# Optimization experiments

Hardware: AMD Instinct MI355X
Metric: run time of the kernel (lower is better)

The kernel has to match this reference:

```python
import jax, jax.numpy as jnp
import numpy as np

N_SAMPLES = 8192
EMBED_DIM = 128
NUM_CLASSES = 100


def setup_inputs() -> dict:
    key = jax.random.key(0)
    k1, k2 = jax.random.split(key)
    x = jax.random.normal(k1, (N_SAMPLES, EMBED_DIM), dtype=jnp.float32)
    # FastAP assumes L2-normalized embeddings (dist2 = 2 - 2*cos in [0, 4])
    x = x / jnp.linalg.norm(x, axis=1, keepdims=True)
    labels = jax.random.randint(k2, (N_SAMPLES,), 0, NUM_CLASSES, dtype=jnp.int64 if jax.config.jax_enable_x64 else jnp.int32)
    return {"batch": x, "labels": labels, "num_bins": 10}


def reference(batch, labels, num_bins):
    N = batch.shape[0]
    L = num_bins + 1                      # number of histogram bin centers (edges of linspace)
    Delta = 4.0 / num_bins                # bin width
    Z = jnp.linspace(0.0, 4.0, L)

    same = labels[:, None] == labels[None, :]
    eye = jnp.eye(N, dtype=bool)
    I_pos = (same & ~eye).astype(batch.dtype)   # Aff > 0
    I_neg = (~same).astype(batch.dtype)         # Aff < 0 (diag is 'same', so excluded)
    N_pos = I_pos.sum(axis=1)

    # squared euclidean distance for unit-norm rows: 2 - 2*cos
    dist2 = 2.0 - 2.0 * (batch @ batch.T)       # [N, N]

    # soft-binning histogram: one N x N pulse per bin, reduced to per-row counts.
    # lax.map keeps only one [N, N] pulse buffer alive at a time.
    def bin_fn(z):
        pulse = jnp.maximum(0.0, 1.0 - jnp.abs(dist2 - z) / Delta)
        return (jnp.einsum('ij,ij->i', pulse, I_pos),
                jnp.einsum('ij,ij->i', pulse, I_neg))

    hp, hn = jax.lax.map(bin_fn, Z)             # each [L, N]
    h_pos = hp.T                                # [N, L]
    h_neg = hn.T

    H_pos = jnp.cumsum(h_pos, axis=1)
    H = jnp.cumsum(h_pos + h_neg, axis=1)

    # FastAP = h_pos * H_pos / H, with NaN/Inf (H == 0) zeroed, as in the original
    safe_H = jnp.where(H > 0, H, 1.0)
    ap = jnp.where(H > 0, h_pos * H_pos / safe_H, 0.0).sum(axis=1)

    # divide by N_pos; rows with no positives are dropped from the mean
    valid = N_pos > 0
    safe_Np = jnp.where(valid, N_pos, 1.0)
    ap = jnp.where(valid, ap / safe_Np, 0.0)

    n_valid = valid.sum().astype(batch.dtype)
    loss = 1.0 - ap.sum() / n_valid
    return loss
```

## Files before the change

kernel.cpp:

```cpp
#include <hip/hip_runtime.h>

#define NS 8192
#define EMBED 128
#define ROWCHUNK 512
#define NPANEL (ROWCHUNK / 32)
#define AROW 12
#define INV64K (1.0f / 65536.0f)

typedef __bf16 bf16x8 __attribute__((ext_vector_type(8)));
typedef float f32x4 __attribute__((ext_vector_type(4)));
typedef float f32x2 __attribute__((ext_vector_type(2)));
typedef const __attribute__((address_space(1))) unsigned ag_u32;
typedef __attribute__((address_space(3))) unsigned al_u32;

#define OFF_XB  0u
#define OFF_GS  2097152u
#define OFF_GSP 2228224u
#define OFF_GA  2359296u
#define OFF_GAP 2752512u
#define OFF_DB  3145728u
#define OFF_AC  3146240u
#define ZERO_BYTES 1049104u

__device__ inline unsigned short f2bf(float f) {
  unsigned u = __float_as_uint(f);
  u += 0x7fffu + ((u >> 16) & 1u);
  return (unsigned short)(u >> 16);
}
__device__ inline float clamp01(float x) { return __builtin_amdgcn_fmed3f(x, 0.f, 1.f); }

__global__ __launch_bounds__(256) void prep_kernel(const float* __restrict__ x,
                                                   unsigned short* __restrict__ xb,
                                                   uint4* __restrict__ zbase) {
  const int gid = blockIdx.x * 256 + threadIdx.x;
  const int row = gid >> 4, g = gid & 15;
  const float4 v0 = reinterpret_cast<const float4*>(x)[row * 32 + g * 2];
  const float4 v1 = reinterpret_cast<const float4*>(x)[row * 32 + g * 2 + 1];
  uint4 o;
  o.x = (unsigned)f2bf(v0.x) | ((unsigned)f2bf(v0.y) << 16);
  o.y = (unsigned)f2bf(v0.z) | ((unsigned)f2bf(v0.w) << 16);
  o.z = (unsigned)f2bf(v1.x) | ((unsigned)f2bf(v1.y) << 16);
  o.w = (unsigned)f2bf(v1.z) | ((unsigned)f2bf(v1.w) << 16);
  reinterpret_cast<uint4*>(xb)[row * 16 + (g ^ (row & 7))] = o;
  if (gid < (int)(ZERO_BYTES / 16u)) zbase[gid] = make_uint4(0u, 0u, 0u, 0u);
}

__global__ __launch_bounds__(256, 8) void fastap_main_kernel(
    const unsigned short* __restrict__ xb,
    const int* __restrict__ labels,
    unsigned* __restrict__ gS, unsigned* __restrict__ gSp,
    unsigned* __restrict__ gA, unsigned* __restrict__ gAp,
    unsigned* __restrict__ doneBx,
    float* __restrict__ accum, unsigned* __restrict__ done,
    float* __restrict__ out) {
  __shared__ __align__(16) unsigned short sA[2][32 * 128];
  __shared__ int sLab[ROWCHUNK];
  __shared__ int sFinal;

  const int tid  = threadIdx.x;
  const int wave = tid >> 6;
  const int lane = tid & 63;
  const int l16  = lane & 15;
  const int quad = lane >> 4;
  const int colBase  = blockIdx.x * 64;
  const int rowChunk = blockIdx.y * ROWCHUNK;

  if (tid < ROWCHUNK / 4)
    reinterpret_cast<int4*>(sLab)[tid] =
        reinterpret_cast<const int4*>(labels + rowChunk)[tid];

  const int jcol = colBase + wave * 16 + l16;
  bf16x8 bfr[4];
  #pragma unroll
  for (int kb = 0; kb < 4; ++kb) {
    const int pg = (kb * 4 + quad) ^ (l16 & 7);
    bfr[kb] = *reinterpret_cast<const bf16x8*>(&xb[jcol * 128 + pg * 8]);
  }
  const int labj = labels[jcol];

  f32x2 C01 = {0.f, 0.f}, C23 = {0.f, 0.f};
  f32x2 Cp01 = {0.f, 0.f}, Cp23 = {0.f, 0.f};

  int aOff[4];
  #pragma unroll
  for (int kb = 0; kb < 4; ++kb)
    aOff[kb] = l16 * 128 + (((kb * 4 + quad) ^ (l16 & 7)) << 3);

  const unsigned short* xrb = xb + rowChunk * 128;
  auto stage = [&](int p, int b) {
    const unsigned short* src = xrb + p * (32 * 128);
    __builtin_amdgcn_global_load_lds((ag_u32*)(src + tid * 8),
                                     (al_u32*)(&sA[b][tid * 8]), 16, 0, 0);
    __builtin_amdgcn_global_load_lds((ag_u32*)(src + (tid + 256) * 8),
                                     (al_u32*)(&sA[b][(tid + 256) * 8]), 16, 0, 0);
  };

  auto tile16 = [&](const unsigned short* ap, int lcr) {
    const int4 lr = *reinterpret_cast<const int4*>(&sLab[lcr + quad * 4]);
    bf16x8 a0 = *reinterpret_cast<const bf16x8*>(&ap[aOff[0]]);
    bf16x8 a1 = *reinterpret_cast<const bf16x8*>(&ap[aOff[1]]);
    bf16x8 a2 = *reinterpret_cast<const bf16x8*>(&ap[aOff[2]]);
    bf16x8 a3 = *reinterpret_cast<const bf16x8*>(&ap[aOff[3]]);
    f32x4 acc = {0.f, 0.f, 0.f, 0.f};
    acc = __builtin_amdgcn_mfma_f32_16x16x32_bf16(a0, bfr[0], acc, 0, 0, 0);
    acc = __builtin_amdgcn_mfma_f32_16x16x32_bf16(a1, bfr[1], acc, 0, 0, 0);
    acc = __builtin_amdgcn_mfma_f32_16x16x32_bf16(a2, bfr[2], acc, 0, 0, 0);
    acc = __builtin_amdgcn_mfma_f32_16x16x32_bf16(a3, bfr[3], acc, 0, 0, 0);

    const int labr[4] = {lr.x, lr.y, lr.z, lr.w};
    #pragma unroll
    for (int r = 0; r < 4; ++r) {
      const float a = acc[r];
      const float pm = (labr[r] == labj) ? 1.f : 0.f;
      const f32x2 av = {a, a}, p2 = {pm, pm};
      f32x2 d01 = __builtin_elementwise_fma(av, (f32x2){5.f, 5.f},
                                            (f32x2){-1.f, 0.f});
      f32x2 d23 = __builtin_elementwise_fma(av, (f32x2){5.f, 5.f},
                                            (f32x2){1.f, 2.f});
      d01 = (f32x2){clamp01(d01.x), clamp01(d01.y)};
      d23 = (f32x2){clamp01(d23.x), clamp01(d23.y)};
      C01 += d01; C23 += d23;
      Cp01 = __builtin_elementwise_fma(p2, d01, Cp01);
      Cp23 = __builtin_elementwise_fma(p2, d23, Cp23);
    }

    const float mabs = fmaxf(fmaxf(fabsf(acc[0]), fabsf(acc[1])),
                             fmaxf(fabsf(acc[2]), fabsf(acc[3])));
    if (__builtin_expect(mabs > 0.4f, 0)) {
      #pragma unroll
      for (int r = 0; r < 4; ++r) {
        const float a = acc[r];
        if (fabsf(a) <= 0.4f) continue;
        const int i = rowChunk + lcr + quad * 4 + r;
        const float d0 = clamp01(fmaf(a, 5.f, -1.f));
        const float d1 = clamp01(a * 5.f);
        const float d2 = clamp01(fmaf(a, 5.f, 1.f));
        const float d3 = clamp01(fmaf(a, 5.f, 2.f));
        if (i == jcol) {
          C01 -= (f32x2){d0, d1};  C23 -= (f32x2){d2, d3};
          Cp01 -= (f32x2){d0, d1}; Cp23 -= (f32x2){d2, d3};
          #pragma unroll
          for (int k = 7; k <= 10; ++k)
            atomicAdd(&gA[jcol * AROW + k], (unsigned)(-65536));
        } else {
          const bool isPos = (labr[r] == labj);
          const float t = fmaf(a, -5.f, 5.f);
          #pragma unroll
          for (int k = 0; k <= 2; ++k) {
            const float v = clamp01((float)(k + 1) - t);
            const int q = (int)(v * 65536.f + 0.5f);
            if (q) {
              atomicAdd(&gA[jcol * AROW + k], (unsigned)q);
              if (isPos) atomicAdd(&gAp[jcol * AROW + k], (unsigned)q);
            }
          }
          #pragma unroll
          for (int k = 7; k <= 10; ++k) {
            const float v = clamp01((float)(k + 1) - t) - 1.f;
            const int q = (int)(v * 65536.f - 0.5f);
            if (q) {
              atomicAdd(&gA[jcol * AROW + k], (unsigned)q);
              if (isPos) atomicAdd(&gAp[jcol * AROW + k], (unsigned)q);
            }
          }
        }
      }
    }
  };

  stage(0, 0);
  __syncthreads();

  #pragma unroll 1
  for (int p = 0; p < NPANEL; ++p) {
    const int cur = p & 1;
    if (p + 1 < NPANEL) stage(p + 1, cur ^ 1);
    tile16(&sA[cur][0],        p * 32);
    tile16(&sA[cur][16 * 128], p * 32 + 16);
    __syncthreads();
  }

  #pragma unroll
  for (int m = 16; m < 64; m <<= 1) {
    C01.x  += __shfl_xor(C01.x,  m, 64); C01.y  += __shfl_xor(C01.y,  m, 64);
    C23.x  += __shfl_xor(C23.x,  m, 64); C23.y  += __shfl_xor(C23.y,  m, 64);
    Cp01.x += __shfl_xor(Cp01.x, m, 64); Cp01.y += __shfl_xor(Cp01.y, m, 64);
    Cp23.x += __shfl_xor(Cp23.x, m, 64); Cp23.y += __shfl_xor(Cp23.y, m, 64);
  }

  if (quad == 0) {
    const float Cv[4]  = {C01.x, C01.y, C23.x, C23.y};
    const float Cpv[4] = {Cp01.x, Cp01.y, Cp23.x, Cp23.y};
    #pragma unroll
    for (int k = 0; k < 4; ++k) {
      atomicAdd(&gS[jcol * 4 + k],  (unsigned)(int)lrintf(Cv[k]  * 65536.f));
      atomicAdd(&gSp[jcol * 4 + k], (unsigned)(int)lrintf(Cpv[k] * 65536.f));
    }
  }

  __syncthreads();
  if (tid == 0) {
    __asm__ volatile("" ::: "memory");
    sFinal = (atomicAdd(&doneBx[blockIdx.x], 1u) == 15u);
  }
  __syncthreads();
  if (!sFinal) return;

  if (tid < 128) sLab[tid] = 0;
  __syncthreads();
  for (int idx = tid; idx < NS; idx += 256)
    atomicAdd(&sLab[labels[idx]], 1);
  __syncthreads();

  if (tid < 64) {
    const int col = colBase + tid;
    const int np = sLab[labels[col]] - 1;

    unsigned gsv[4], gspv[4], gav[11], gapv[11];
    #pragma unroll
    for (int k = 0; k < 4; ++k) {
      gsv[k]  = atomicAdd(&gS[col * 4 + k], 0u);
      gspv[k] = atomicAdd(&gSp[col * 4 + k], 0u);
    }
    #pragma unroll
    for (int b = 0; b < 11; ++b) {
      gav[b]  = atomicAdd(&gA[col * AROW + b], 0u);
      gapv[b] = atomicAdd(&gAp[col * AROW + b], 0u);
    }

    float ap = 0.f, val = 0.f, HpPrev = 0.f;
    #pragma unroll
    for (int b = 0; b <= 10; ++b) {
      const float baseH  = (b < 3) ? 0.f
                         : (b < 7) ? (float)(int)gsv[b - 3]  * INV64K : 8192.f;
      const float basePp = (b < 3) ? 0.f
                         : (b < 7) ? (float)(int)gspv[b - 3] * INV64K : (float)np;
      const float H  = baseH  + (float)(int)gav[b]  * INV64K;
      const float Hp = basePp + (float)(int)gapv[b] * INV64K;
      const float hp = Hp - HpPrev;
      HpPrev = Hp;
      if (H > 1e-6f) ap += hp * Hp / H;
    }
    if (np > 0) { ap /= (float)np; val = 1.f; } else ap = 0.f;

    #pragma unroll
    for (int m = 1; m < 64; m <<= 1) {
      ap  += __shfl_xor(ap,  m, 64);
      val += __shfl_xor(val, m, 64);
    }
    if (tid == 0) {
      atomicAdd(&accum[0], ap);
      atomicAdd(&accum[1], val);
      __builtin_amdgcn_s_waitcnt(0);
      __asm__ volatile("" ::: "memory");
      const unsigned prev = atomicAdd(done, 1u);
      if (prev == 127u) {
        const float a2 = atomicAdd(&accum[0], 0.f);
        const float c2 = atomicAdd(&accum[1], 0.f);
        out[0] = 1.f - (c2 > 0.f ? a2 / c2 : 0.f);
      }
    }
  }
}

extern "C" void kernel_launch(void* const* d_in, const int* in_sizes, int n_in,
                              void* d_out, int out_size, void* d_ws, size_t ws_size,
                              hipStream_t stream) {
  const float* x      = (const float*)d_in[0];
  const int*   labels = (const int*)d_in[1];
  float* out = (float*)d_out;

  char* ws = (char*)d_ws;
  unsigned short* xb = (unsigned short*)(ws + OFF_XB);
  unsigned* gS    = (unsigned*)(ws + OFF_GS);
  unsigned* gSp   = (unsigned*)(ws + OFF_GSP);
  unsigned* gA    = (unsigned*)(ws + OFF_GA);
  unsigned* gAp   = (unsigned*)(ws + OFF_GAP);
  unsigned* dBx   = (unsigned*)(ws + OFF_DB);
  float*    accum = (float*)(ws + OFF_AC);
  unsigned* done  = (unsigned*)(ws + OFF_AC + 8);

  prep_kernel<<<512, 256, 0, stream>>>(x, xb, (uint4*)(ws + OFF_GS));
  fastap_main_kernel<<<dim3(NS / 64, NS / ROWCHUNK), 256, 0, stream>>>(
      xb, labels, gS, gSp, gA, gAp, dBx, accum, done, out);
}
```

Baseline: 113.8 us.

## Replace global atomics for cumulative sums with per-rowchunk partial stores

Each block now writes its per-column cumulative bin partials as plain 8-byte stores into a per-row-chunk slot. The last block for a column group sums the 16 slots itself, so the integer atomic accumulation is gone. Per-column-block label counts are built in shared memory during the main loop and added into a small global table, which removes the final block's full 8192-label histogram pass. Finalization loads become relaxed atomic loads instead of atomicAdd(0). The cost is a larger workspace and 16 extra loads per column in the tail.

```diff
diff --git a/kernel.cpp b/kernel.cpp
--- a/kernel.cpp
+++ b/kernel.cpp
@@ -15,12 +15,13 @@
 
 #define OFF_XB  0u
 #define OFF_GS  2097152u
-#define OFF_GSP 2228224u
-#define OFF_GA  2359296u
-#define OFF_GAP 2752512u
-#define OFF_DB  3145728u
-#define OFF_AC  3146240u
-#define ZERO_BYTES 1049104u
+#define OFF_GSP 4194304u
+#define OFF_GA  6291456u
+#define OFF_GAP 6684672u
+#define OFF_CS  7077888u
+#define OFF_DB  7143424u
+#define OFF_AC  7143936u
+#define ZERO_BYTES 852496u
 
 __device__ inline unsigned short f2bf(float f) {
   unsigned u = __float_as_uint(f);
@@ -28,6 +29,23 @@
   return (unsigned short)(u >> 16);
 }
 __device__ inline float clamp01(float x) { return __builtin_amdgcn_fmed3f(x, 0.f, 1.f); }
+
+__device__ inline void st8_dev(float* p, float x, float y) {
+  unsigned long long u =
+      ((unsigned long long)__float_as_uint(y) << 32) | __float_as_uint(x);
+  __hip_atomic_store(reinterpret_cast<unsigned long long*>(p), u,
+                     __ATOMIC_RELAXED, __HIP_MEMORY_SCOPE_AGENT);
+}
+__device__ inline float2 ld8_dev(const float* p) {
+  unsigned long long u =
+      __hip_atomic_load(reinterpret_cast<const unsigned long long*>(p),
+                        __ATOMIC_RELAXED, __HIP_MEMORY_SCOPE_AGENT);
+  return make_float2(__uint_as_float((unsigned)u),
+                     __uint_as_float((unsigned)(u >> 32)));
+}
+__device__ inline unsigned ld4_dev(const unsigned* p) {
+  return __hip_atomic_load(p, __ATOMIC_RELAXED, __HIP_MEMORY_SCOPE_AGENT);
+}
 
 __global__ __launch_bounds__(256) void prep_kernel(const float* __restrict__ x,
                                                    unsigned short* __restrict__ xb,
@@ -48,13 +66,14 @@
 __global__ __launch_bounds__(256, 8) void fastap_main_kernel(
     const unsigned short* __restrict__ xb,
     const int* __restrict__ labels,
-    unsigned* __restrict__ gS, unsigned* __restrict__ gSp,
+    float* __restrict__ gS, float* __restrict__ gSp,
     unsigned* __restrict__ gA, unsigned* __restrict__ gAp,
-    unsigned* __restrict__ doneBx,
+    unsigned* __restrict__ ccS, unsigned* __restrict__ doneBx,
     float* __restrict__ accum, unsigned* __restrict__ done,
     float* __restrict__ out) {
   __shared__ __align__(16) unsigned short sA[2][32 * 128];
   __shared__ int sLab[ROWCHUNK];
+  __shared__ int sHist[128];
   __shared__ int sFinal;
 
   const int tid  = threadIdx.x;
@@ -65,6 +84,7 @@
   const int colBase  = blockIdx.x * 64;
   const int rowChunk = blockIdx.y * ROWCHUNK;
 
+  if (tid < 128) sHist[tid] = 0;
   if (tid < ROWCHUNK / 4)
     reinterpret_cast<int4*>(sLab)[tid] =
         reinterpret_cast<const int4*>(labels + rowChunk)[tid];
@@ -171,6 +191,9 @@
   stage(0, 0);
   __syncthreads();
 
+  atomicAdd(&sHist[sLab[tid]], 1);
+  atomicAdd(&sHist[sLab[tid + 256]], 1);
+
   #pragma unroll 1
   for (int p = 0; p < NPANEL; ++p) {
     const int cur = p & 1;
@@ -180,6 +203,9 @@
     __syncthreads();
   }
 
+  if (tid < 128 && sHist[tid])
+    atomicAdd(&ccS[blockIdx.x * 128 + tid], (unsigned)sHist[tid]);
+
   #pragma unroll
   for (int m = 16; m < 64; m <<= 1) {
     C01.x  += __shfl_xor(C01.x,  m, 64); C01.y  += __shfl_xor(C01.y,  m, 64);
@@ -189,52 +215,47 @@
   }
 
   if (quad == 0) {
-    const float Cv[4]  = {C01.x, C01.y, C23.x, C23.y};
-    const float Cpv[4] = {Cp01.x, Cp01.y, Cp23.x, Cp23.y};
-    #pragma unroll
-    for (int k = 0; k < 4; ++k) {
-      atomicAdd(&gS[jcol * 4 + k],  (unsigned)(int)lrintf(Cv[k]  * 65536.f));
-      atomicAdd(&gSp[jcol * 4 + k], (unsigned)(int)lrintf(Cpv[k] * 65536.f));
-    }
+    float* b1 = gS  + (unsigned)(blockIdx.y * NS + jcol) * 4u;
+    float* b2 = gSp + (unsigned)(blockIdx.y * NS + jcol) * 4u;
+    st8_dev(b1,     C01.x,  C01.y);
+    st8_dev(b1 + 2, C23.x,  C23.y);
+    st8_dev(b2,     Cp01.x, Cp01.y);
+    st8_dev(b2 + 2, Cp23.x, Cp23.y);
   }
 
   __syncthreads();
-  if (tid == 0) {
-    __asm__ volatile("" ::: "memory");
+  if (tid == 0)
     sFinal = (atomicAdd(&doneBx[blockIdx.x], 1u) == 15u);
-  }
   __syncthreads();
   if (!sFinal) return;
 
-  if (tid < 128) sLab[tid] = 0;
-  __syncthreads();
-  for (int idx = tid; idx < NS; idx += 256)
-    atomicAdd(&sLab[labels[idx]], 1);
-  __syncthreads();
-
   if (tid < 64) {
     const int col = colBase + tid;
-    const int np = sLab[labels[col]] - 1;
-
-    unsigned gsv[4], gspv[4], gav[11], gapv[11];
-    #pragma unroll
-    for (int k = 0; k < 4; ++k) {
-      gsv[k]  = atomicAdd(&gS[col * 4 + k], 0u);
-      gspv[k] = atomicAdd(&gSp[col * 4 + k], 0u);
-    }
+    const int np = (int)ld4_dev(&ccS[blockIdx.x * 128 + labels[col]]) - 1;
+
+    float Cs[4]  = {0.f, 0.f, 0.f, 0.f};
+    float Cps[4] = {0.f, 0.f, 0.f, 0.f};
+    #pragma unroll 4
+    for (int s = 0; s < 16; ++s) {
+      const float* b1 = gS  + (unsigned)(s * NS + col) * 4u;
+      const float* b2 = gSp + (unsigned)(s * NS + col) * 4u;
+      const float2 u0 = ld8_dev(b1), u1 = ld8_dev(b1 + 2);
+      const float2 v0 = ld8_dev(b2), v1 = ld8_dev(b2 + 2);
+      Cs[0]  += u0.x; Cs[1]  += u0.y; Cs[2]  += u1.x; Cs[3]  += u1.y;
+      Cps[0] += v0.x; Cps[1] += v0.y; Cps[2] += v1.x; Cps[3] += v1.y;
+    }
+    unsigned gav[11], gapv[11];
     #pragma unroll
     for (int b = 0; b < 11; ++b) {
-      gav[b]  = atomicAdd(&gA[col * AROW + b], 0u);
-      gapv[b] = atomicAdd(&gAp[col * AROW + b], 0u);
+      gav[b]  = ld4_dev(&gA[col * AROW + b]);
+      gapv[b] = ld4_dev(&gAp[col * AROW + b]);
     }
 
     float ap = 0.f, val = 0.f, HpPrev = 0.f;
     #pragma unroll
     for (int b = 0; b <= 10; ++b) {
-      const float baseH  = (b < 3) ? 0.f
-                         : (b < 7) ? (float)(int)gsv[b - 3]  * INV64K : 8192.f;
-      const float basePp = (b < 3) ? 0.f
-                         : (b < 7) ? (float)(int)gspv[b - 3] * INV64K : (float)np;
+      const float baseH  = (b < 3) ? 0.f : (b < 7) ? Cs[b - 3]  : 8192.f;
+      const float basePp = (b < 3) ? 0.f : (b < 7) ? Cps[b - 3] : (float)np;
       const float H  = baseH  + (float)(int)gav[b]  * INV64K;
       const float Hp = basePp + (float)(int)gapv[b] * INV64K;
       const float hp = Hp - HpPrev;
@@ -272,15 +293,16 @@
 
   char* ws = (char*)d_ws;
   unsigned short* xb = (unsigned short*)(ws + OFF_XB);
-  unsigned* gS    = (unsigned*)(ws + OFF_GS);
-  unsigned* gSp   = (unsigned*)(ws + OFF_GSP);
+  float*    gS    = (float*)(ws + OFF_GS);
+  float*    gSp   = (float*)(ws + OFF_GSP);
   unsigned* gA    = (unsigned*)(ws + OFF_GA);
   unsigned* gAp   = (unsigned*)(ws + OFF_GAP);
+  unsigned* ccS   = (unsigned*)(ws + OFF_CS);
   unsigned* dBx   = (unsigned*)(ws + OFF_DB);
   float*    accum = (float*)(ws + OFF_AC);
   unsigned* done  = (unsigned*)(ws + OFF_AC + 8);
 
-  prep_kernel<<<512, 256, 0, stream>>>(x, xb, (uint4*)(ws + OFF_GS));
+  prep_kernel<<<512, 256, 0, stream>>>(x, xb, (uint4*)(ws + OFF_GA));
   fastap_main_kernel<<<dim3(NS / 64, NS / ROWCHUNK), 256, 0, stream>>>(
-      xb, labels, gS, gSp, gA, gAp, dBx, accum, done, out);
-}
+      xb, labels, gS, gSp, gA, gAp, ccS, dBx, accum, done, out);
+}
```

Measured after the change: 112.5 us. About the same (-1.2%).
